# Kernel tuning notes

Hardware: AMD Instinct MI355X
Metric: run time of the kernel (lower is better)

## Reference

```python
import jax, jax.numpy as jnp
import numpy as np

N_NODES = 100000
N_EDGES = 3200000
D_IN = 64
D_HID = 64


def _gcn_conv(h, src, dst, norm, W, b, n_nodes):
    # h: [N, d_in] -> linear transform first (as in PyG GCNConv)
    h = h @ W  # [N, d_out]
    msg = h[src] * norm[:, None]  # gather + scale, [E', d_out]
    out = jax.ops.segment_sum(msg, dst, num_segments=n_nodes)  # scatter-add
    return out + b


def setup_inputs() -> dict:
    key = jax.random.key(0)
    k1, k2, k3, k4 = jax.random.split(key, 4)
    x = jax.random.normal(k1, (N_NODES, D_IN), dtype=jnp.float32)
    edge_index = jax.random.randint(k2, (2, N_EDGES), 0, N_NODES, dtype=jnp.int64)
    # Glorot-style init for linear weights, zero bias (PyG defaults)
    W1 = jax.random.normal(k3, (D_IN, D_HID), dtype=jnp.float32) * (1.0 / np.sqrt(D_IN))
    b1 = jnp.zeros((D_HID,), dtype=jnp.float32)
    W2 = jax.random.normal(k4, (D_HID, D_HID), dtype=jnp.float32) * (1.0 / np.sqrt(D_HID))
    b2 = jnp.zeros((D_HID,), dtype=jnp.float32)
    return {"x": x, "edge_index": edge_index, "W1": W1, "b1": b1, "W2": W2, "b2": b2}


def reference(x, edge_index, W1, b1, W2, b2):
    n = x.shape[0]
    # add self-loops (PyG GCNConv default add_self_loops=True)
    loops = jnp.arange(n, dtype=edge_index.dtype)
    src = jnp.concatenate([edge_index[0], loops])  # [E + N]
    dst = jnp.concatenate([edge_index[1], loops])
    # symmetric normalization: deg over destination (in-degree incl. self-loop)
    deg = jax.ops.segment_sum(jnp.ones_like(src, dtype=x.dtype), dst, num_segments=n)
    deg_inv_sqrt = jnp.where(deg > 0, jax.lax.rsqrt(jnp.maximum(deg, 1.0)), 0.0)
    norm = deg_inv_sqrt[src] * deg_inv_sqrt[dst]  # [E + N]

    h = _gcn_conv(x, src, dst, norm, W1, b1, n)
    h = jax.nn.relu(h)
    out = _gcn_conv(h, src, dst, norm, W2, b2, n)
    return out
```

## Files before the change

### kernel.cpp

```cpp
#include <hip/hip_runtime.h>

typedef unsigned short ushort_t;
typedef unsigned int uint_t;

#define SCAN_CHUNK 1024
#define NCH 256
#define BSHIFT 8
#define BNODES 256
#define MAXNB 512

__device__ __forceinline__ ushort_t f32_to_bf16(float f) {
    uint_t u = __float_as_uint(f);
    return (ushort_t)((u + 0x7FFF + ((u >> 16) & 1)) >> 16);
}
__device__ __forceinline__ float bf16_to_f32(ushort_t h) {
    return __uint_as_float((uint_t)h << 16);
}


__global__ __launch_bounds__(256) void chunk_hist_kernel(const int* __restrict__ dst,
                                                         int* __restrict__ histG,
                                                         int E, int NB, int chunk) {
    __shared__ int lh[MAXNB];
    int c = blockIdx.x;
    for (int i = threadIdx.x; i < NB; i += 256) lh[i] = 0;
    __syncthreads();
    int beg = c * chunk, end = min(beg + chunk, E);
    for (int e = beg + threadIdx.x; e < end; e += 256) atomicAdd(&lh[dst[e] >> BSHIFT], 1);
    __syncthreads();
    for (int i = threadIdx.x; i < NB; i += 256) histG[i * NCH + c] = lh[i];
}


__global__ void block_sum_kernel(const int* __restrict__ in, int* __restrict__ partials, int L) {
    __shared__ int sdata[256];
    int base = blockIdx.x * SCAN_CHUNK;
    int sum = 0;
    for (int i = threadIdx.x; i < SCAN_CHUNK; i += 256) {
        int idx = base + i;
        sum += (idx < L) ? in[idx] : 0;
    }
    sdata[threadIdx.x] = sum;
    __syncthreads();
    for (int s = 128; s > 0; s >>= 1) {
        if (threadIdx.x < s) sdata[threadIdx.x] += sdata[threadIdx.x + s];
        __syncthreads();
    }
    if (threadIdx.x == 0) partials[blockIdx.x] = sdata[0];
}

__global__ void scan_partials_kernel(int* __restrict__ partials, int nb,
                                     int* __restrict__ out, int L) {
    if (threadIdx.x == 0 && blockIdx.x == 0) {
        int acc = 0;
        for (int i = 0; i < nb; i++) { int v = partials[i]; partials[i] = acc; acc += v; }
        out[L] = acc;
    }
}

__global__ void scan_write_kernel(const int* __restrict__ in, const int* __restrict__ partials,
                                  int* __restrict__ out, int L) {
    __shared__ int sdata[256];
    int base = blockIdx.x * SCAN_CHUNK;
    int tbase = base + threadIdx.x * 4;
    int vals[4];
    int tsum = 0;
    #pragma unroll
    for (int j = 0; j < 4; j++) {
        int idx = tbase + j;
        vals[j] = (idx < L) ? in[idx] : 0;
        tsum += vals[j];
    }
    sdata[threadIdx.x] = tsum;
    __syncthreads();
    for (int s = 1; s < 256; s <<= 1) {
        int v = (threadIdx.x >= s) ? sdata[threadIdx.x - s] : 0;
        __syncthreads();
        sdata[threadIdx.x] += v;
        __syncthreads();
    }
    int excl = (threadIdx.x == 0) ? 0 : sdata[threadIdx.x - 1];
    int offset = partials[blockIdx.x] + excl;
    #pragma unroll
    for (int j = 0; j < 4; j++) {
        int idx = tbase + j;
        if (idx < L) out[idx] = offset;
        offset += vals[j];
    }
}


__global__ __launch_bounds__(256) void chunk_scatter_kernel(const int* __restrict__ src,
                                                            const int* __restrict__ dst,
                                                            const int* __restrict__ histBase,
                                                            int* __restrict__ binned,
                                                            int E, int NB, int chunk) {
    __shared__ int cur[MAXNB];
    int c = blockIdx.x;
    for (int i = threadIdx.x; i < NB; i += 256) cur[i] = histBase[i * NCH + c];
    __syncthreads();
    int beg = c * chunk, end = min(beg + chunk, E);
    for (int e = beg + threadIdx.x; e < end; e += 256) {
        int s = src[e], d = dst[e];
        int pos = atomicAdd(&cur[d >> BSHIFT], 1);
        binned[pos] = s | ((d & (BNODES - 1)) << 24);
    }
}


__global__ __launch_bounds__(256) void bucket_finalize_kernel(const int* __restrict__ binned,
                                                              const int* __restrict__ histBase,
                                                              int* __restrict__ row_ptr,
                                                              float* __restrict__ dinv,
                                                              int* __restrict__ srcidx, int n) {
    __shared__ int cl[BNODES];
    __shared__ int sl[BNODES];
    int b = blockIdx.x;
    int tid = threadIdx.x;
    cl[tid] = 0;
    __syncthreads();
    int beg = histBase[b * NCH], end = histBase[(b + 1) * NCH];
    for (int e = beg + tid; e < end; e += 256)
        atomicAdd(&cl[(uint_t)binned[e] >> 24], 1);
    __syncthreads();
    int mycnt = cl[tid];
    sl[tid] = mycnt;
    __syncthreads();
    for (int s = 1; s < 256; s <<= 1) {
        int v = (tid >= s) ? sl[tid - s] : 0;
        __syncthreads();
        sl[tid] += v;
        __syncthreads();
    }
    int excl = tid ? sl[tid - 1] : 0;
    int myrp = beg + excl;
    cl[tid] = myrp;
    int node = (b << BSHIFT) + tid;
    if (node < n) {
        row_ptr[node] = myrp;
        dinv[node] = rsqrtf((float)(mycnt + 1));
        if (node == n - 1) row_ptr[n] = myrp + mycnt;
    }
    __syncthreads();
    for (int e = beg + tid; e < end; e += 256) {
        int v = binned[e];
        int pos = atomicAdd(&cl[(uint_t)v >> 24], 1);
        srcidx[pos] = v & 0xFFFFFF;
    }
}


__global__ __launch_bounds__(256) void transform_kernel(const float* __restrict__ in,
                                                        const float* __restrict__ W,
                                                        const float* __restrict__ dinv,
                                                        ushort_t* __restrict__ g, int n) {
    __shared__ float xs[4 * 256];
    int lane = threadIdx.x & 63;
    int wslot = threadIdx.x >> 6;
    float* myxs = &xs[wslot * 256];

    float wreg[64];
    #pragma unroll
    for (int k = 0; k < 64; k++) wreg[k] = W[k * 64 + lane];

    int wave = (blockIdx.x * 256 + threadIdx.x) >> 6;
    int nwaves = gridDim.x * 4;
    int ngroups = (n + 3) >> 2;
    for (int grp = wave; grp < ngroups; grp += nwaves) {
        int r0 = grp * 4;
        if (r0 + 4 <= n) {
            float4 xv = *reinterpret_cast<const float4*>(&in[(size_t)r0 * 64 + lane * 4]);
            *reinterpret_cast<float4*>(&myxs[lane * 4]) = xv;
            float acc0 = 0.f, acc1 = 0.f, acc2 = 0.f, acc3 = 0.f;
            #pragma unroll
            for (int k4 = 0; k4 < 16; k4++) {
                float4 a = *reinterpret_cast<const float4*>(&myxs[0 * 64 + k4 * 4]);
                float4 b = *reinterpret_cast<const float4*>(&myxs[1 * 64 + k4 * 4]);
                float4 c = *reinterpret_cast<const float4*>(&myxs[2 * 64 + k4 * 4]);
                float4 d = *reinterpret_cast<const float4*>(&myxs[3 * 64 + k4 * 4]);
                float w0 = wreg[k4 * 4 + 0], w1 = wreg[k4 * 4 + 1];
                float w2 = wreg[k4 * 4 + 2], w3 = wreg[k4 * 4 + 3];
                acc0 = fmaf(a.x, w0, acc0); acc0 = fmaf(a.y, w1, acc0);
                acc0 = fmaf(a.z, w2, acc0); acc0 = fmaf(a.w, w3, acc0);
                acc1 = fmaf(b.x, w0, acc1); acc1 = fmaf(b.y, w1, acc1);
                acc1 = fmaf(b.z, w2, acc1); acc1 = fmaf(b.w, w3, acc1);
                acc2 = fmaf(c.x, w0, acc2); acc2 = fmaf(c.y, w1, acc2);
                acc2 = fmaf(c.z, w2, acc2); acc2 = fmaf(c.w, w3, acc2);
                acc3 = fmaf(d.x, w0, acc3); acc3 = fmaf(d.y, w1, acc3);
                acc3 = fmaf(d.z, w2, acc3); acc3 = fmaf(d.w, w3, acc3);
            }
            g[(size_t)(r0 + 0) * 64 + lane] = f32_to_bf16(acc0 * dinv[r0 + 0]);
            g[(size_t)(r0 + 1) * 64 + lane] = f32_to_bf16(acc1 * dinv[r0 + 1]);
            g[(size_t)(r0 + 2) * 64 + lane] = f32_to_bf16(acc2 * dinv[r0 + 2]);
            g[(size_t)(r0 + 3) * 64 + lane] = f32_to_bf16(acc3 * dinv[r0 + 3]);
        } else {
            for (int r = r0; r < n; r++) {
                float acc = 0.f;
                #pragma unroll
                for (int k = 0; k < 64; k++) acc = fmaf(in[(size_t)r * 64 + k], wreg[k], acc);
                g[(size_t)r * 64 + lane] = f32_to_bf16(acc * dinv[r]);
            }
        }
    }
}


__global__ __launch_bounds__(256) void aggregate_kernel(const ushort_t* __restrict__ g,
                                                        const int* __restrict__ row_ptr,
                                                        const int* __restrict__ srcidx,
                                                        const float* __restrict__ dinv,
                                                        const float* __restrict__ b,
                                                        float* __restrict__ out, int n, int relu) {
    int lane = threadIdx.x & 63;
    int node = (blockIdx.x * 256 + threadIdx.x) >> 6;
    if (node >= n) return;
    node = __builtin_amdgcn_readfirstlane(node);
    int beg = row_ptr[node];
    int end = row_ptr[node + 1];
    float acc = bf16_to_f32(g[(size_t)node * 64 + lane]);
    int e = beg;
    for (; e + 8 <= end; e += 8) {
        int s0 = srcidx[e + 0], s1 = srcidx[e + 1], s2 = srcidx[e + 2], s3 = srcidx[e + 3];
        int s4 = srcidx[e + 4], s5 = srcidx[e + 5], s6 = srcidx[e + 6], s7 = srcidx[e + 7];
        float v0 = bf16_to_f32(g[(size_t)s0 * 64 + lane]);
        float v1 = bf16_to_f32(g[(size_t)s1 * 64 + lane]);
        float v2 = bf16_to_f32(g[(size_t)s2 * 64 + lane]);
        float v3 = bf16_to_f32(g[(size_t)s3 * 64 + lane]);
        float v4 = bf16_to_f32(g[(size_t)s4 * 64 + lane]);
        float v5 = bf16_to_f32(g[(size_t)s5 * 64 + lane]);
        float v6 = bf16_to_f32(g[(size_t)s6 * 64 + lane]);
        float v7 = bf16_to_f32(g[(size_t)s7 * 64 + lane]);
        acc += ((v0 + v1) + (v2 + v3)) + ((v4 + v5) + (v6 + v7));
    }
    for (; e < end; ++e) acc += bf16_to_f32(g[(size_t)srcidx[e] * 64 + lane]);
    float o = fmaf(dinv[node], acc, b[lane]);
    out[(size_t)node * 64 + lane] = relu ? fmaxf(o, 0.f) : o;
}

extern "C" void kernel_launch(void* const* d_in, const int* in_sizes, int n_in,
                              void* d_out, int out_size, void* d_ws, size_t ws_size,
                              hipStream_t stream) {
    const float* x  = (const float*)d_in[0];
    const int*   ei = (const int*)d_in[1];
    const float* W1 = (const float*)d_in[2];
    const float* b1 = (const float*)d_in[3];
    const float* W2 = (const float*)d_in[4];
    const float* b2 = (const float*)d_in[5];
    float* out = (float*)d_out;

    const int n = in_sizes[0] / 64;
    const int E = in_sizes[1] / 2;
    const int* src = ei;
    const int* dst = ei + E;
    const int NB = (n + BNODES - 1) >> BSHIFT;
    const int chunk = (E + NCH - 1) / NCH;
    const int L = NB * NCH;

    char* ws = (char*)d_ws;
    size_t off = 0;
    auto carve = [&](size_t bytes) { char* p = ws + off; off = (off + bytes + 255) & ~(size_t)255; return p; };
    int*      row_ptr  = (int*)     carve((size_t)(n + 1) * 4);
    int*      partials = (int*)     carve(4096);
    float*    dinv     = (float*)   carve((size_t)n * 4);
    int*      histG    = (int*)     carve((size_t)L * 4);
    int*      histBase = (int*)     carve((size_t)(L + 1) * 4);
    int*      srcidx   = (int*)     carve((size_t)E * 4);
    int*      binned   = (int*)     carve((size_t)E * 4);
    ushort_t* g        = (ushort_t*)carve((size_t)n * 64 * 2);

    const int nbs_hist = (L + SCAN_CHUNK - 1) / SCAN_CHUNK;

    chunk_hist_kernel<<<NCH, 256, 0, stream>>>(dst, histG, E, NB, chunk);
    block_sum_kernel<<<nbs_hist, 256, 0, stream>>>(histG, partials, L);
    scan_partials_kernel<<<1, 64, 0, stream>>>(partials, nbs_hist, histBase, L);
    scan_write_kernel<<<nbs_hist, 256, 0, stream>>>(histG, partials, histBase, L);
    chunk_scatter_kernel<<<NCH, 256, 0, stream>>>(src, dst, histBase, binned, E, NB, chunk);
    bucket_finalize_kernel<<<NB, 256, 0, stream>>>(binned, histBase, row_ptr, dinv, srcidx, n);

    const int agg_grid = (n * 64 + 255) / 256;

    transform_kernel<<<2048, 256, 0, stream>>>(x, W1, dinv, g, n);
    aggregate_kernel<<<agg_grid, 256, 0, stream>>>(g, row_ptr, srcidx, dinv, b1, out, n, 1);

    transform_kernel<<<2048, 256, 0, stream>>>(out, W2, dinv, g, n);
    aggregate_kernel<<<agg_grid, 256, 0, stream>>>(g, row_ptr, srcidx, dinv, b2, out, n, 0);
}
```

Baseline: 273.0 us.

## Partition CSR edges by source slice for cache-local gathers in aggregation

The bucket finalize now sorts each node's incoming edges by source-node slice (16384 nodes per slice) and writes a per-slice row pointer array. The aggregation kernel launches a fixed grid in which each wave owns 25 nodes. It walks the slices in an outer loop so concurrent gathers fall in a roughly 2MB window of the feature table, aiming for better L2 reuse. The histogram and scatter kernels also read src/dst with int4 vector loads. The trade-offs are fewer edges per inner loop, more row-pointer traffic, less parallelism per node, and no cross-wave coordination to keep waves on the same slice.

```diff
diff --git a/kernel.cpp b/kernel.cpp
--- a/kernel.cpp
+++ b/kernel.cpp
@@ -8,6 +8,10 @@
 #define BSHIFT 8
 #define BNODES 256
 #define MAXNB 512
+#define SLICE_SHIFT 14
+#define MAXP 8
+#define AGG_BLOCKS 1024
+#define NV 25
 
 __device__ __forceinline__ ushort_t f32_to_bf16(float f) {
     uint_t u = __float_as_uint(f);
@@ -26,7 +30,15 @@
     for (int i = threadIdx.x; i < NB; i += 256) lh[i] = 0;
     __syncthreads();
     int beg = c * chunk, end = min(beg + chunk, E);
-    for (int e = beg + threadIdx.x; e < end; e += 256) atomicAdd(&lh[dst[e] >> BSHIFT], 1);
+    int e = beg + threadIdx.x * 4;
+    for (; e + 4 <= end; e += 1024) {
+        int4 d4 = *reinterpret_cast<const int4*>(&dst[e]);
+        atomicAdd(&lh[d4.x >> BSHIFT], 1);
+        atomicAdd(&lh[d4.y >> BSHIFT], 1);
+        atomicAdd(&lh[d4.z >> BSHIFT], 1);
+        atomicAdd(&lh[d4.w >> BSHIFT], 1);
+    }
+    for (; e < end; ++e) atomicAdd(&lh[dst[e] >> BSHIFT], 1);
     __syncthreads();
     for (int i = threadIdx.x; i < NB; i += 256) histG[i * NCH + c] = lh[i];
 }
@@ -100,7 +112,20 @@
     for (int i = threadIdx.x; i < NB; i += 256) cur[i] = histBase[i * NCH + c];
     __syncthreads();
     int beg = c * chunk, end = min(beg + chunk, E);
-    for (int e = beg + threadIdx.x; e < end; e += 256) {
+    int e = beg + threadIdx.x * 4;
+    for (; e + 4 <= end; e += 1024) {
+        int4 s4 = *reinterpret_cast<const int4*>(&src[e]);
+        int4 d4 = *reinterpret_cast<const int4*>(&dst[e]);
+        int p0 = atomicAdd(&cur[d4.x >> BSHIFT], 1);
+        binned[p0] = s4.x | ((d4.x & (BNODES - 1)) << 24);
+        int p1 = atomicAdd(&cur[d4.y >> BSHIFT], 1);
+        binned[p1] = s4.y | ((d4.y & (BNODES - 1)) << 24);
+        int p2 = atomicAdd(&cur[d4.z >> BSHIFT], 1);
+        binned[p2] = s4.z | ((d4.z & (BNODES - 1)) << 24);
+        int p3 = atomicAdd(&cur[d4.w >> BSHIFT], 1);
+        binned[p3] = s4.w | ((d4.w & (BNODES - 1)) << 24);
+    }
+    for (; e < end; ++e) {
         int s = src[e], d = dst[e];
         int pos = atomicAdd(&cur[d >> BSHIFT], 1);
         binned[pos] = s | ((d & (BNODES - 1)) << 24);
@@ -110,20 +135,27 @@
 
 __global__ __launch_bounds__(256) void bucket_finalize_kernel(const int* __restrict__ binned,
                                                               const int* __restrict__ histBase,
-                                                              int* __restrict__ row_ptr,
+                                                              int* __restrict__ row_ptr2,
                                                               float* __restrict__ dinv,
-                                                              int* __restrict__ srcidx, int n) {
-    __shared__ int cl[BNODES];
+                                                              int* __restrict__ srcidx,
+                                                              int n, int P) {
+    __shared__ int cl[BNODES * MAXP];
     __shared__ int sl[BNODES];
     int b = blockIdx.x;
     int tid = threadIdx.x;
-    cl[tid] = 0;
+    for (int j = tid; j < BNODES * P; j += 256) cl[j] = 0;
     __syncthreads();
     int beg = histBase[b * NCH], end = histBase[(b + 1) * NCH];
-    for (int e = beg + tid; e < end; e += 256)
-        atomicAdd(&cl[(uint_t)binned[e] >> 24], 1);
-    __syncthreads();
-    int mycnt = cl[tid];
+    for (int e = beg + tid; e < end; e += 256) {
+        int v = binned[e];
+        int s = v & 0xFFFFFF;
+        int l = (uint_t)v >> 24;
+        atomicAdd(&cl[l * P + (s >> SLICE_SHIFT)], 1);
+    }
+    __syncthreads();
+    int myc[MAXP];
+    int mycnt = 0;
+    for (int p = 0; p < P; p++) { myc[p] = cl[tid * P + p]; mycnt += myc[p]; }
     sl[tid] = mycnt;
     __syncthreads();
     for (int s = 1; s < 256; s <<= 1) {
@@ -133,19 +165,24 @@
         __syncthreads();
     }
     int excl = tid ? sl[tid - 1] : 0;
-    int myrp = beg + excl;
-    cl[tid] = myrp;
     int node = (b << BSHIFT) + tid;
+    int run = beg + excl;
+    for (int p = 0; p < P; p++) {
+        cl[tid * P + p] = run;
+        if (node < n) row_ptr2[node * P + p] = run;
+        run += myc[p];
+    }
     if (node < n) {
-        row_ptr[node] = myrp;
         dinv[node] = rsqrtf((float)(mycnt + 1));
-        if (node == n - 1) row_ptr[n] = myrp + mycnt;
+        if (node == n - 1) row_ptr2[n * P] = run;
     }
     __syncthreads();
     for (int e = beg + tid; e < end; e += 256) {
         int v = binned[e];
-        int pos = atomicAdd(&cl[(uint_t)v >> 24], 1);
-        srcidx[pos] = v & 0xFFFFFF;
+        int s = v & 0xFFFFFF;
+        int l = (uint_t)v >> 24;
+        int pos = atomicAdd(&cl[l * P + (s >> SLICE_SHIFT)], 1);
+        srcidx[pos] = s;
     }
 }
 
@@ -205,36 +242,52 @@
 }
 
 
-__global__ __launch_bounds__(256) void aggregate_kernel(const ushort_t* __restrict__ g,
-                                                        const int* __restrict__ row_ptr,
-                                                        const int* __restrict__ srcidx,
-                                                        const float* __restrict__ dinv,
-                                                        const float* __restrict__ b,
-                                                        float* __restrict__ out, int n, int relu) {
+__global__ __launch_bounds__(256, 4) void aggregate_kernel(const ushort_t* __restrict__ g,
+                                                           const int* __restrict__ row_ptr2,
+                                                           const int* __restrict__ srcidx,
+                                                           const float* __restrict__ dinv,
+                                                           const float* __restrict__ bias,
+                                                           float* __restrict__ out,
+                                                           int n, int P, int relu) {
     int lane = threadIdx.x & 63;
-    int node = (blockIdx.x * 256 + threadIdx.x) >> 6;
-    if (node >= n) return;
-    node = __builtin_amdgcn_readfirstlane(node);
-    int beg = row_ptr[node];
-    int end = row_ptr[node + 1];
-    float acc = bf16_to_f32(g[(size_t)node * 64 + lane]);
-    int e = beg;
-    for (; e + 8 <= end; e += 8) {
-        int s0 = srcidx[e + 0], s1 = srcidx[e + 1], s2 = srcidx[e + 2], s3 = srcidx[e + 3];
-        int s4 = srcidx[e + 4], s5 = srcidx[e + 5], s6 = srcidx[e + 6], s7 = srcidx[e + 7];
-        float v0 = bf16_to_f32(g[(size_t)s0 * 64 + lane]);
-        float v1 = bf16_to_f32(g[(size_t)s1 * 64 + lane]);
-        float v2 = bf16_to_f32(g[(size_t)s2 * 64 + lane]);
-        float v3 = bf16_to_f32(g[(size_t)s3 * 64 + lane]);
-        float v4 = bf16_to_f32(g[(size_t)s4 * 64 + lane]);
-        float v5 = bf16_to_f32(g[(size_t)s5 * 64 + lane]);
-        float v6 = bf16_to_f32(g[(size_t)s6 * 64 + lane]);
-        float v7 = bf16_to_f32(g[(size_t)s7 * 64 + lane]);
-        acc += ((v0 + v1) + (v2 + v3)) + ((v4 + v5) + (v6 + v7));
-    }
-    for (; e < end; ++e) acc += bf16_to_f32(g[(size_t)srcidx[e] * 64 + lane]);
-    float o = fmaf(dinv[node], acc, b[lane]);
-    out[(size_t)node * 64 + lane] = relu ? fmaxf(o, 0.f) : o;
+    int wave = (blockIdx.x * 256 + threadIdx.x) >> 6;
+    const int NW = AGG_BLOCKS * 4;
+
+    float acc[NV];
+    #pragma unroll
+    for (int k = 0; k < NV; k++) {
+        int node = wave + k * NW;
+        acc[k] = (node < n) ? bf16_to_f32(g[(size_t)node * 64 + lane]) : 0.f;
+    }
+    for (int p = 0; p < P; p++) {
+        #pragma unroll
+        for (int k = 0; k < NV; k++) {
+            int node = wave + k * NW;
+            if (node >= n) continue;
+            int e = row_ptr2[node * P + p];
+            int e1 = row_ptr2[node * P + p + 1];
+            float a = acc[k];
+            for (; e + 4 <= e1; e += 4) {
+                int s0 = srcidx[e + 0], s1 = srcidx[e + 1];
+                int s2 = srcidx[e + 2], s3 = srcidx[e + 3];
+                float v0 = bf16_to_f32(g[(size_t)s0 * 64 + lane]);
+                float v1 = bf16_to_f32(g[(size_t)s1 * 64 + lane]);
+                float v2 = bf16_to_f32(g[(size_t)s2 * 64 + lane]);
+                float v3 = bf16_to_f32(g[(size_t)s3 * 64 + lane]);
+                a += (v0 + v1) + (v2 + v3);
+            }
+            for (; e < e1; ++e) a += bf16_to_f32(g[(size_t)srcidx[e] * 64 + lane]);
+            acc[k] = a;
+        }
+    }
+    float bl = bias[lane];
+    #pragma unroll
+    for (int k = 0; k < NV; k++) {
+        int node = wave + k * NW;
+        if (node >= n) continue;
+        float o = fmaf(dinv[node], acc[k], bl);
+        out[(size_t)node * 64 + lane] = relu ? fmaxf(o, 0.f) : o;
+    }
 }
 
 extern "C" void kernel_launch(void* const* d_in, const int* in_sizes, int n_in,
@@ -255,15 +308,16 @@
     const int NB = (n + BNODES - 1) >> BSHIFT;
     const int chunk = (E + NCH - 1) / NCH;
     const int L = NB * NCH;
+    const int P = (n + (1 << SLICE_SHIFT) - 1) >> SLICE_SHIFT;
 
     char* ws = (char*)d_ws;
     size_t off = 0;
     auto carve = [&](size_t bytes) { char* p = ws + off; off = (off + bytes + 255) & ~(size_t)255; return p; };
-    int*      row_ptr  = (int*)     carve((size_t)(n + 1) * 4);
     int*      partials = (int*)     carve(4096);
     float*    dinv     = (float*)   carve((size_t)n * 4);
     int*      histG    = (int*)     carve((size_t)L * 4);
     int*      histBase = (int*)     carve((size_t)(L + 1) * 4);
+    int*      row_ptr2 = (int*)     carve(((size_t)n * MAXP + 1) * 4);
     int*      srcidx   = (int*)     carve((size_t)E * 4);
     int*      binned   = (int*)     carve((size_t)E * 4);
     ushort_t* g        = (ushort_t*)carve((size_t)n * 64 * 2);
@@ -275,13 +329,11 @@
     scan_partials_kernel<<<1, 64, 0, stream>>>(partials, nbs_hist, histBase, L);
     scan_write_kernel<<<nbs_hist, 256, 0, stream>>>(histG, partials, histBase, L);
     chunk_scatter_kernel<<<NCH, 256, 0, stream>>>(src, dst, histBase, binned, E, NB, chunk);
-    bucket_finalize_kernel<<<NB, 256, 0, stream>>>(binned, histBase, row_ptr, dinv, srcidx, n);
-
-    const int agg_grid = (n * 64 + 255) / 256;
+    bucket_finalize_kernel<<<NB, 256, 0, stream>>>(binned, histBase, row_ptr2, dinv, srcidx, n, P);
 
     transform_kernel<<<2048, 256, 0, stream>>>(x, W1, dinv, g, n);
-    aggregate_kernel<<<agg_grid, 256, 0, stream>>>(g, row_ptr, srcidx, dinv, b1, out, n, 1);
+    aggregate_kernel<<<AGG_BLOCKS, 256, 0, stream>>>(g, row_ptr2, srcidx, dinv, b1, out, n, P, 1);
 
     transform_kernel<<<2048, 256, 0, stream>>>(out, W2, dinv, g, n);
-    aggregate_kernel<<<agg_grid, 256, 0, stream>>>(g, row_ptr, srcidx, dinv, b2, out, n, 0);
-}
+    aggregate_kernel<<<AGG_BLOCKS, 256, 0, stream>>>(g, row_ptr2, srcidx, dinv, b2, out, n, P, 0);
+}
```

After: 679.0 us. +148.8%, slower.

## Split aggregation by feature quarter across edge groups; vectorize binning loads

Applied to the files above, without the earlier changes.

The aggregation kernel now assigns each wavefront one node and a 16-column quarter of the features. Its four 16-lane groups process different edges in parallel and are then combined with cross-lane shuffles. The grid interleaves quarters so neighbouring blocks share the same nodes. The aim is more independent gathers in flight per wave and better spread of per-node work. The histogram and scatter binning kernels also load src/dst as int4 to cut load instructions, which assumes 16-byte alignment of chunk starts, and each gather now touches only 32 bytes per row.

```diff
diff --git a/kernel.cpp b/kernel.cpp
--- a/kernel.cpp
+++ b/kernel.cpp
@@ -26,7 +26,15 @@
     for (int i = threadIdx.x; i < NB; i += 256) lh[i] = 0;
     __syncthreads();
     int beg = c * chunk, end = min(beg + chunk, E);
-    for (int e = beg + threadIdx.x; e < end; e += 256) atomicAdd(&lh[dst[e] >> BSHIFT], 1);
+    int e = beg + threadIdx.x * 4;
+    for (; e + 4 <= end; e += 1024) {
+        int4 d4 = *reinterpret_cast<const int4*>(&dst[e]);
+        atomicAdd(&lh[d4.x >> BSHIFT], 1);
+        atomicAdd(&lh[d4.y >> BSHIFT], 1);
+        atomicAdd(&lh[d4.z >> BSHIFT], 1);
+        atomicAdd(&lh[d4.w >> BSHIFT], 1);
+    }
+    for (; e < end; ++e) atomicAdd(&lh[dst[e] >> BSHIFT], 1);
     __syncthreads();
     for (int i = threadIdx.x; i < NB; i += 256) histG[i * NCH + c] = lh[i];
 }
@@ -100,7 +108,20 @@
     for (int i = threadIdx.x; i < NB; i += 256) cur[i] = histBase[i * NCH + c];
     __syncthreads();
     int beg = c * chunk, end = min(beg + chunk, E);
-    for (int e = beg + threadIdx.x; e < end; e += 256) {
+    int e = beg + threadIdx.x * 4;
+    for (; e + 4 <= end; e += 1024) {
+        int4 s4 = *reinterpret_cast<const int4*>(&src[e]);
+        int4 d4 = *reinterpret_cast<const int4*>(&dst[e]);
+        int p0 = atomicAdd(&cur[d4.x >> BSHIFT], 1);
+        binned[p0] = s4.x | ((d4.x & (BNODES - 1)) << 24);
+        int p1 = atomicAdd(&cur[d4.y >> BSHIFT], 1);
+        binned[p1] = s4.y | ((d4.y & (BNODES - 1)) << 24);
+        int p2 = atomicAdd(&cur[d4.z >> BSHIFT], 1);
+        binned[p2] = s4.z | ((d4.z & (BNODES - 1)) << 24);
+        int p3 = atomicAdd(&cur[d4.w >> BSHIFT], 1);
+        binned[p3] = s4.w | ((d4.w & (BNODES - 1)) << 24);
+    }
+    for (; e < end; ++e) {
         int s = src[e], d = dst[e];
         int pos = atomicAdd(&cur[d >> BSHIFT], 1);
         binned[pos] = s | ((d & (BNODES - 1)) << 24);
@@ -205,36 +226,53 @@
 }
 
 
-__global__ __launch_bounds__(256) void aggregate_kernel(const ushort_t* __restrict__ g,
-                                                        const int* __restrict__ row_ptr,
-                                                        const int* __restrict__ srcidx,
-                                                        const float* __restrict__ dinv,
-                                                        const float* __restrict__ b,
-                                                        float* __restrict__ out, int n, int relu) {
+__global__ __launch_bounds__(256) void aggregate_q_kernel(const ushort_t* __restrict__ g,
+                                                          const int* __restrict__ row_ptr,
+                                                          const int* __restrict__ srcidx,
+                                                          const float* __restrict__ dinv,
+                                                          const float* __restrict__ bias,
+                                                          float* __restrict__ out,
+                                                          int n, int relu) {
     int lane = threadIdx.x & 63;
-    int node = (blockIdx.x * 256 + threadIdx.x) >> 6;
+    int wv = threadIdx.x >> 6;
+    int grp = lane >> 4;
+    int f = lane & 15;
+    int q = (blockIdx.x & 7) >> 1;
+    int nb = ((blockIdx.x >> 3) << 1) + (blockIdx.x & 1);
+    int node = nb * 4 + wv;
     if (node >= n) return;
     node = __builtin_amdgcn_readfirstlane(node);
-    int beg = row_ptr[node];
-    int end = row_ptr[node + 1];
-    float acc = bf16_to_f32(g[(size_t)node * 64 + lane]);
-    int e = beg;
-    for (; e + 8 <= end; e += 8) {
-        int s0 = srcidx[e + 0], s1 = srcidx[e + 1], s2 = srcidx[e + 2], s3 = srcidx[e + 3];
-        int s4 = srcidx[e + 4], s5 = srcidx[e + 5], s6 = srcidx[e + 6], s7 = srcidx[e + 7];
-        float v0 = bf16_to_f32(g[(size_t)s0 * 64 + lane]);
-        float v1 = bf16_to_f32(g[(size_t)s1 * 64 + lane]);
-        float v2 = bf16_to_f32(g[(size_t)s2 * 64 + lane]);
-        float v3 = bf16_to_f32(g[(size_t)s3 * 64 + lane]);
-        float v4 = bf16_to_f32(g[(size_t)s4 * 64 + lane]);
-        float v5 = bf16_to_f32(g[(size_t)s5 * 64 + lane]);
-        float v6 = bf16_to_f32(g[(size_t)s6 * 64 + lane]);
-        float v7 = bf16_to_f32(g[(size_t)s7 * 64 + lane]);
-        acc += ((v0 + v1) + (v2 + v3)) + ((v4 + v5) + (v6 + v7));
-    }
-    for (; e < end; ++e) acc += bf16_to_f32(g[(size_t)srcidx[e] * 64 + lane]);
-    float o = fmaf(dinv[node], acc, b[lane]);
-    out[(size_t)node * 64 + lane] = relu ? fmaxf(o, 0.f) : o;
+    int col = (q << 4) + f;
+
+    int e0 = row_ptr[node];
+    int e1 = row_ptr[node + 1];
+    float acc = (grp == 0) ? bf16_to_f32(g[(size_t)node * 64 + col]) : 0.f;
+    int e = e0;
+    for (; e + 16 <= e1; e += 16) {
+        int sA = srcidx[e + grp];
+        int sB = srcidx[e + 4 + grp];
+        int sC = srcidx[e + 8 + grp];
+        int sD = srcidx[e + 12 + grp];
+        float vA = bf16_to_f32(g[(size_t)sA * 64 + col]);
+        float vB = bf16_to_f32(g[(size_t)sB * 64 + col]);
+        float vC = bf16_to_f32(g[(size_t)sC * 64 + col]);
+        float vD = bf16_to_f32(g[(size_t)sD * 64 + col]);
+        acc += (vA + vB) + (vC + vD);
+    }
+    for (; e + 4 <= e1; e += 4) {
+        int s = srcidx[e + grp];
+        acc += bf16_to_f32(g[(size_t)s * 64 + col]);
+    }
+    if (e + grp < e1) {
+        int s = srcidx[e + grp];
+        acc += bf16_to_f32(g[(size_t)s * 64 + col]);
+    }
+    acc += __shfl_xor(acc, 16, 64);
+    acc += __shfl_xor(acc, 32, 64);
+    if (grp == 0) {
+        float o = fmaf(dinv[node], acc, bias[col]);
+        out[(size_t)node * 64 + col] = relu ? fmaxf(o, 0.f) : o;
+    }
 }
 
 extern "C" void kernel_launch(void* const* d_in, const int* in_sizes, int n_in,
@@ -277,11 +315,12 @@
     chunk_scatter_kernel<<<NCH, 256, 0, stream>>>(src, dst, histBase, binned, E, NB, chunk);
     bucket_finalize_kernel<<<NB, 256, 0, stream>>>(binned, histBase, row_ptr, dinv, srcidx, n);
 
-    const int agg_grid = (n * 64 + 255) / 256;
+    const int ngrp4 = (n + 3) / 4;
+    const int aggB = ((ngrp4 + 1) / 2) * 8;
 
     transform_kernel<<<2048, 256, 0, stream>>>(x, W1, dinv, g, n);
-    aggregate_kernel<<<agg_grid, 256, 0, stream>>>(g, row_ptr, srcidx, dinv, b1, out, n, 1);
+    aggregate_q_kernel<<<aggB, 256, 0, stream>>>(g, row_ptr, srcidx, dinv, b1, out, n, 1);
 
     transform_kernel<<<2048, 256, 0, stream>>>(out, W2, dinv, g, n);
-    aggregate_kernel<<<agg_grid, 256, 0, stream>>>(g, row_ptr, srcidx, dinv, b2, out, n, 0);
-}
+    aggregate_q_kernel<<<aggB, 256, 0, stream>>>(g, row_ptr, srcidx, dinv, b2, out, n, 0);
+}
```

Result: slower. 547.1 us (+100.4%).
